# Performance work log

Measured on AMD Instinct MI355X. Metric: run time of the kernel, lower is better.

The kernel has to match this reference:

```python
import jax, jax.numpy as jnp
import numpy as np

L, H, D, HD, DFF, V, S, B = 12, 12, 768, 64, 3072, 50257, 512, 4
NEG = -1e10  # mask value used by the torch module (applied incl. diagonal, pre-scale)


def layer_norm(x, g, b, eps=1e-5):
    u = jnp.mean(x, axis=-1, keepdims=True)
    v = jnp.mean((x - u) ** 2, axis=-1, keepdims=True)  # biased variance
    return g * (x - u) / jnp.sqrt(v + eps) + b


def setup_inputs() -> dict:
    key = jax.random.key(0)
    ks = jax.random.split(key, 10)
    f = lambda k, s: 0.02 * jax.random.normal(k, s, dtype=jnp.float32)
    return {
        "tokens": jax.random.randint(ks[0], (B, S), 0, V),
        "E": f(ks[1], (V, D)),
        "P": f(ks[2], (S, D)),
        "Wq": f(ks[3], (L, H, HD, D)),
        "Wk": f(ks[4], (L, H, HD, D)),
        "Wv": f(ks[5], (L, H, HD, D)),
        "Wo": f(ks[6], (L, D, D)),
        "bo": jnp.zeros((L, D), jnp.float32),
        "g1": jnp.ones((L, D), jnp.float32),
        "b1": jnp.zeros((L, D), jnp.float32),
        "g2": jnp.ones((L, D), jnp.float32),
        "b2": jnp.zeros((L, D), jnp.float32),
        "W1": f(ks[7], (L, DFF, D)),
        "bff1": jnp.zeros((L, DFF), jnp.float32),
        "W2": f(ks[8], (L, D, DFF)),
        "bff2": jnp.zeros((L, D), jnp.float32),
        "gf": jnp.ones((D,), jnp.float32),
        "bf": jnp.zeros((D,), jnp.float32),
    }


def reference(tokens, E, P, Wq, Wk, Wv, Wo, bo, g1, b1, g2, b2, W1, bff1, W2, bff2, gf, bf):
    x = E[tokens] + P[None, :, :]  # [B,S,D]; embed_dropout is identity at eval
    # Faithful mask: triu with diagonal=0 (masks the diagonal too), added BEFORE 1/sqrt(dk)
    mask = jnp.triu(jnp.ones((S, S), jnp.float32), k=0) * NEG
    scale = 1.0 / jnp.sqrt(jnp.float32(HD))
    for l in range(L):
        h = layer_norm(x, g1[l], b1[l])
        Q = jnp.einsum('bsd,hkd->bhsk', h, Wq[l])
        K = jnp.einsum('bsd,hkd->bhsk', h, Wk[l])
        Vh = jnp.einsum('bsd,hkd->bhsk', h, Wv[l])
        sc = (jnp.einsum('bhqk,bhmk->bhqm', Q, K) + mask) * scale  # [B,H,S,S]
        A = jax.nn.softmax(sc, axis=-1)
        o = jnp.einsum('bhqm,bhmk->bhqk', A, Vh)  # [B,H,S,HD]
        o = o.transpose(0, 2, 1, 3).reshape(B, S, D)  # concat heads
        x = x + jnp.einsum('bsd,ed->bse', o, Wo[l]) + bo[l]
        h2 = layer_norm(x, g2[l], b2[l])
        ff = jax.nn.gelu(jnp.einsum('bsd,fd->bsf', h2, W1[l]) + bff1[l], approximate=False)
        x = x + jnp.einsum('bsf,df->bsd', ff, W2[l]) + bff2[l]
    x = layer_norm(x, gf, bf)
    return jnp.einsum('bsd,vd->bsv', x, E)  # weight-tied LM head
```

## Files before the change

### kernel.cpp

```cpp
#include <hip/hip_runtime.h>
#include <hip/hip_bf16.h>
#include <math.h>
#include <stdint.h>

#define L      12
#define H      12
#define DMODEL 768
#define HDIM   64
#define DFF    3072
#define VOCAB  50257
#define VPAD2  50432
#define SEQ    512
#define BATCH  4
#define MTOK   2048
#define BKK    64

typedef __hip_bfloat16 bf16;
typedef __bf16 bf16x8 __attribute__((ext_vector_type(8)));
typedef float  f32x4  __attribute__((ext_vector_type(4)));

__device__ inline unsigned int f2bf_bits(float f) {
    __hip_bfloat16 h = __float2bfloat16(f);
    return (unsigned int)__builtin_bit_cast(unsigned short, h);
}

typedef __attribute__((address_space(1))) unsigned int as1_uint;
typedef __attribute__((address_space(3))) unsigned int as3_uint;

__device__ inline void load_lds_16B(const void* g, void* l) {
    __builtin_amdgcn_global_load_lds((as1_uint*)(uintptr_t)g,
                                     (as3_uint*)(uintptr_t)l, 16, 0, 0);
}

__device__ inline int xcd_swz(int raw, int nwg) {
    return (raw & 7) * (nwg >> 3) + (raw >> 3);
}

struct CvtP {
    const float* src[7];
    bf16* dst[7];
    long ns[7];
    long nt[7];
};

__global__ void cvt_all_kernel(CvtP c) {
    long gid0 = ((long)blockIdx.x * blockDim.x + threadIdx.x) * 8;
    long gstr = (long)gridDim.x * blockDim.x * 8;
    for (int s = 0; s < 7; s++) {
        const float* src = c.src[s];
        bf16* dst = c.dst[s];
        long ns = c.ns[s], ntt = c.nt[s];
        for (long i8 = gid0; i8 < ntt; i8 += gstr) {
            uint4 out;
            if (i8 < ns) {
                float4 a = *reinterpret_cast<const float4*>(src + i8);
                float4 b = *reinterpret_cast<const float4*>(src + i8 + 4);
                out.x = f2bf_bits(a.x) | (f2bf_bits(a.y) << 16);
                out.y = f2bf_bits(a.z) | (f2bf_bits(a.w) << 16);
                out.z = f2bf_bits(b.x) | (f2bf_bits(b.y) << 16);
                out.w = f2bf_bits(b.z) | (f2bf_bits(b.w) << 16);
            } else {
                out = (uint4){0u, 0u, 0u, 0u};
            }
            *reinterpret_cast<uint4*>(dst + i8) = out;
        }
    }
}

__global__ __launch_bounds__(256) void embed_ln_kernel(
        float* __restrict__ x, bf16* __restrict__ hout,
        const int* __restrict__ tok, const float* __restrict__ E,
        const float* __restrict__ Pp, const float* __restrict__ g,
        const float* __restrict__ b) {
    int wave = threadIdx.x >> 6, lane = threadIdx.x & 63;
    int row = blockIdx.x * 4 + wave;
    int s = row & (SEQ - 1);
    long ebase = (long)tok[row] * 192;
    const float4* E4 = (const float4*)E;
    const float4* P4 = (const float4*)Pp;
    float4 v[3];
    float s1 = 0.f, s2 = 0.f;
    #pragma unroll
    for (int e = 0; e < 3; e++) {
        int c4 = e * 64 + lane;
        float4 a = E4[ebase + c4];
        float4 p = P4[s * 192 + c4];
        a.x += p.x; a.y += p.y; a.z += p.z; a.w += p.w;
        v[e] = a;
        ((float4*)x)[(size_t)row * 192 + c4] = a;
        s1 += a.x + a.y + a.z + a.w;
        s2 += a.x * a.x + a.y * a.y + a.z * a.z + a.w * a.w;
    }
    #pragma unroll
    for (int o = 32; o > 0; o >>= 1) {
        s1 += __shfl_xor(s1, o);
        s2 += __shfl_xor(s2, o);
    }
    float u    = s1 * (1.f / DMODEL);
    float var  = s2 * (1.f / DMODEL) - u * u;
    float rstd = rsqrtf(var + 1e-5f);
    #pragma unroll
    for (int e = 0; e < 3; e++) {
        int c4 = e * 64 + lane;
        float4 gg = ((const float4*)g)[c4];
        float4 bb = ((const float4*)b)[c4];
        float y0 = gg.x * (v[e].x - u) * rstd + bb.x;
        float y1 = gg.y * (v[e].y - u) * rstd + bb.y;
        float y2 = gg.z * (v[e].z - u) * rstd + bb.z;
        float y3 = gg.w * (v[e].w - u) * rstd + bb.w;
        uint2 o2;
        o2.x = f2bf_bits(y0) | (f2bf_bits(y1) << 16);
        o2.y = f2bf_bits(y2) | (f2bf_bits(y3) << 16);
        ((uint2*)hout)[(size_t)row * 192 + c4] = o2;
    }
}

__global__ __launch_bounds__(256) void reduce_ln_kernel(
        float* __restrict__ x, const float* __restrict__ part, int S,
        const float* __restrict__ bias, const float* __restrict__ g,
        const float* __restrict__ b, bf16* __restrict__ hout) {
    int wave = threadIdx.x >> 6, lane = threadIdx.x & 63;
    int row = blockIdx.x * 4 + wave;
    const float4* part4 = (const float4*)part;
    float4 v[3];
    float s1 = 0.f, s2 = 0.f;
    #pragma unroll
    for (int e = 0; e < 3; e++) {
        int c4 = e * 64 + lane;
        size_t idx = (size_t)row * 192 + c4;
        float4 a = ((const float4*)x)[idx];
        float4 bi = ((const float4*)bias)[c4];
        a.x += bi.x; a.y += bi.y; a.z += bi.z; a.w += bi.w;
        for (int sl = 0; sl < S; sl++) {
            float4 p = part4[((size_t)sl * MTOK + row) * 192 + c4];
            a.x += p.x; a.y += p.y; a.z += p.z; a.w += p.w;
        }
        v[e] = a;
        ((float4*)x)[idx] = a;
        s1 += a.x + a.y + a.z + a.w;
        s2 += a.x * a.x + a.y * a.y + a.z * a.z + a.w * a.w;
    }
    #pragma unroll
    for (int o = 32; o > 0; o >>= 1) {
        s1 += __shfl_xor(s1, o);
        s2 += __shfl_xor(s2, o);
    }
    float u    = s1 * (1.f / DMODEL);
    float var  = s2 * (1.f / DMODEL) - u * u;
    float rstd = rsqrtf(var + 1e-5f);
    #pragma unroll
    for (int e = 0; e < 3; e++) {
        int c4 = e * 64 + lane;
        float4 gg = ((const float4*)g)[c4];
        float4 bb = ((const float4*)b)[c4];
        float y0 = gg.x * (v[e].x - u) * rstd + bb.x;
        float y1 = gg.y * (v[e].y - u) * rstd + bb.y;
        float y2 = gg.z * (v[e].z - u) * rstd + bb.z;
        float y3 = gg.w * (v[e].w - u) * rstd + bb.w;
        uint2 o2;
        o2.x = f2bf_bits(y0) | (f2bf_bits(y1) << 16);
        o2.y = f2bf_bits(y2) | (f2bf_bits(y3) << 16);
        ((uint2*)hout)[(size_t)row * 192 + c4] = o2;
    }
}

#define BM 128

template<int BN_, int EPI>
__global__ __launch_bounds__(256) void gemm_bt(
    const bf16* __restrict__ A, const bf16* __restrict__ Bmat, long strideBz,
    void* __restrict__ Cout, long strideCz,
    const float* __restrict__ bias,
    int Mm, int Nn, int Kk, int Nstore, int kslice)
{
    constexpr int NF = BN_ / 32;
    __shared__ __align__(16) bf16 As[2][BM * BKK];
    __shared__ __align__(16) bf16 Bs[2][BN_ * BKK];
    int tid = threadIdx.x;
    int lane = tid & 63, wave = tid >> 6;

    int Mtiles = Mm / BM;
    int id = xcd_swz(blockIdx.x, gridDim.x);
    int bm = (id % Mtiles) * BM;
    int bn = (id / Mtiles) * BN_;
    int z = blockIdx.z;
    const bf16* Bz = Bmat + (size_t)z * strideBz;
    int wr = (wave >> 1) * 64, wc = (wave & 1) * (BN_ / 2);

    int k0 = (EPI == 4) ? z * kslice : 0;
    int nt = ((EPI == 4) ? kslice : Kk) / BKK;

    f32x4 acc[4][NF];
    #pragma unroll
    for (int i = 0; i < 4; i++)
        #pragma unroll
        for (int j = 0; j < NF; j++) acc[i][j] = (f32x4){0.f, 0.f, 0.f, 0.f};

    auto stage = [&](int slot, int kt) {
        #pragma unroll
        for (int i = 0; i < 4; i++) {
            int byte = i * 4096 + tid * 16;
            int r = byte >> 7;
            int scb = (byte & 127) ^ ((r & 7) << 4);
            load_lds_16B(A + (size_t)(bm + r) * Kk + kt + (scb >> 1),
                         (char*)As[slot] + byte);
        }
        #pragma unroll
        for (int i = 0; i < BN_ / 32; i++) {
            int byte = i * 4096 + tid * 16;
            int r = byte >> 7;
            int scb = (byte & 127) ^ ((r & 7) << 4);
            load_lds_16B(Bz + (size_t)(bn + r) * Kk + kt + (scb >> 1),
                         (char*)Bs[slot] + byte);
        }
    };

    const int swz_rd = (lane & 7) << 4;
    stage(0, k0);
    for (int t = 0; t < nt; ++t) {
        if (t + 1 < nt) {
            stage((t + 1) & 1, k0 + (t + 1) * BKK);
            if constexpr (BN_ == 128) {
                asm volatile("s_waitcnt vmcnt(8)" ::: "memory");
            } else {
                asm volatile("s_waitcnt vmcnt(6)" ::: "memory");
            }
        } else {
            asm volatile("s_waitcnt vmcnt(0)" ::: "memory");
        }
        __builtin_amdgcn_s_barrier();
        __builtin_amdgcn_sched_barrier(0);
        __builtin_amdgcn_s_setprio(1);
        int cur = t & 1;
        #pragma unroll
        for (int kk = 0; kk < 2; ++kk) {
            bf16x8 af[4], bfr[NF];
            int ro = lane & 15;
            int cob = kk * 64 + (lane >> 4) * 16;
            #pragma unroll
            for (int mi = 0; mi < 4; mi++) {
                int row = wr + mi * 16 + ro;
                af[mi] = *reinterpret_cast<const bf16x8*>(
                    (const char*)As[cur] + row * 128 + (cob ^ swz_rd));
            }
            #pragma unroll
            for (int ni = 0; ni < NF; ni++) {
                int row = wc + ni * 16 + ro;
                bfr[ni] = *reinterpret_cast<const bf16x8*>(
                    (const char*)Bs[cur] + row * 128 + (cob ^ swz_rd));
            }
            #pragma unroll
            for (int mi = 0; mi < 4; mi++)
                #pragma unroll
                for (int ni = 0; ni < NF; ni++)
                    acc[mi][ni] = __builtin_amdgcn_mfma_f32_16x16x32_bf16(
                        af[mi], bfr[ni], acc[mi][ni], 0, 0, 0);
        }
        __builtin_amdgcn_s_setprio(0);
        __builtin_amdgcn_s_barrier();
    }

    int rbase = bm + wr + ((lane >> 4) << 2);
    int cbase = bn + wc + (lane & 15);
    #pragma unroll
    for (int mi = 0; mi < 4; mi++) {
        #pragma unroll
        for (int ni = 0; ni < NF; ni++) {
            int col = cbase + ni * 16;
            #pragma unroll
            for (int r = 0; r < 4; r++) {
                int row = rbase + mi * 16 + r;
                float v = acc[mi][ni][r];
                if constexpr (EPI == 0) {
                    ((bf16*)Cout)[(size_t)z * strideCz + (size_t)row * Nn + col] =
                        __float2bfloat16(v);
                } else if constexpr (EPI == 2) {
                    float t2 = v + bias[col];
                    float gel = 0.5f * t2 * (1.f + erff(t2 * 0.70710678118654752f));
                    ((bf16*)Cout)[(size_t)row * Nn + col] = __float2bfloat16(gel);
                } else if constexpr (EPI == 3) {
                    if (col < Nstore)
                        ((float*)Cout)[(size_t)row * Nstore + col] = v;
                } else {
                    ((float*)Cout)[(size_t)z * strideCz + (size_t)row * Nn + col] = v;
                }
            }
        }
    }
}

#define H8P_READ_A(mq_)                                                        \
    _Pragma("unroll")                                                          \
    for (int mi = 0; mi < 4; mi++) {                                           \
        int row = wm * 64 + mi * 16 + ro;                                      \
        _Pragma("unroll")                                                      \
        for (int kk = 0; kk < 2; kk++) {                                       \
            af[mq_][mi][kk] = *reinterpret_cast<const bf16x8*>(                \
                smem + (slot * 2 + mq_) * 16384 + row * 128 +                  \
                ((kk * 64 + cg16) ^ ((row & 7) << 4)));                        \
        }                                                                      \
    }

#define H8P_READ_B(nq_)                                                       \
    _Pragma("unroll")                                                          \
    for (int ni = 0; ni < 2; ni++) {                                           \
        int row = wn * 32 + ni * 16 + ro;                                      \
        _Pragma("unroll")                                                      \
        for (int kk = 0; kk < 2; kk++) {                                       \
            bfr[nq_][ni][kk] = *reinterpret_cast<const bf16x8*>(               \
                smem + 65536 + (slot * 2 + nq_) * 16384 + row * 128 +          \
                ((kk * 64 + cg16) ^ ((row & 7) << 4)));                        \
        }                                                                      \
    }

#define H8P_MFMA(mq_, nq_)                                                     \
    __builtin_amdgcn_s_setprio(1);                                             \
    _Pragma("unroll")                                                          \
    for (int kk = 0; kk < 2; kk++)                                             \
        _Pragma("unroll")                                                      \
        for (int mi = 0; mi < 4; mi++)                                         \
            _Pragma("unroll")                                                  \
            for (int ni = 0; ni < 2; ni++)                                     \
                acc[mq_][nq_][mi][ni] = __builtin_amdgcn_mfma_f32_16x16x32_bf16( \
                    af[mq_][mi][kk], bfr[nq_][ni][kk], acc[mq_][nq_][mi][ni],  \
                    0, 0, 0);                                                  \
    __builtin_amdgcn_s_setprio(0);

__global__ void __launch_bounds__(512, 2) gemm_head8p(
    const bf16* __restrict__ A, const bf16* __restrict__ Bmat,
    float* __restrict__ Cout, int Nstore)
{
    extern __shared__ char smem[];
    const int Kk = DMODEL;
    const int nt = Kk / BKK;
    int tid = threadIdx.x;
    int lane = tid & 63, wave = tid >> 6;
    int wm = wave >> 2, wn = wave & 3;
    int id = xcd_swz(blockIdx.x, gridDim.x);
    int bm = (id & 7) * 256;
    int bn = (id >> 3) * 256;
    const int ro = lane & 15;
    const int cg16 = (lane >> 4) * 16;

    f32x4 acc[2][2][4][2];
    #pragma unroll
    for (int a0 = 0; a0 < 2; a0++)
        #pragma unroll
        for (int a1 = 0; a1 < 2; a1++)
            #pragma unroll
            for (int a2 = 0; a2 < 4; a2++)
                #pragma unroll
                for (int a3 = 0; a3 < 2; a3++)
                    acc[a0][a1][a2][a3] = (f32x4){0.f, 0.f, 0.f, 0.f};

    bf16x8 af[2][4][2];
    bf16x8 bfr[2][2][2];

    auto stage_half = [&](int slot_, int kt, int which) {
        int h = which >> 1;
        #pragma unroll
        for (int i = 0; i < 2; i++) {
            int byte = i * 8192 + tid * 16;
            int r = byte >> 7;
            int scb = (byte & 127) ^ ((r & 7) << 4);
            if ((which & 1) == 0)
                load_lds_16B(A + (size_t)(bm + h * 128 + r) * Kk + kt + (scb >> 1),
                             smem + (slot_ * 2 + h) * 16384 + byte);
            else
                load_lds_16B(Bmat + (size_t)(bn + h * 128 + r) * Kk + kt + (scb >> 1),
                             smem + 65536 + (slot_ * 2 + h) * 16384 + byte);
        }
    };

    stage_half(0, 0, 0); stage_half(0, 0, 1); stage_half(0, 0, 2); stage_half(0, 0, 3);

    for (int k = 0; k < nt; ++k) {
        int slot = k & 1, nslot = slot ^ 1;
        int kt2 = (k + 1) * BKK;
        bool pf = (k + 1 < nt);

        asm volatile("s_waitcnt vmcnt(4)" ::: "memory");
        if (pf) stage_half(nslot, kt2, 0);
        __builtin_amdgcn_s_barrier();
        __builtin_amdgcn_sched_barrier(0);
        H8P_READ_A(0)
        H8P_READ_B(0)
        asm volatile("s_waitcnt lgkmcnt(0)" ::: "memory");
        __builtin_amdgcn_sched_barrier(0);
        H8P_MFMA(0, 0)

        if (pf) {
            asm volatile("s_waitcnt vmcnt(4)" ::: "memory");
        } else {
            asm volatile("s_waitcnt vmcnt(2)" ::: "memory");
        }
        if (pf) stage_half(nslot, kt2, 1);
        __builtin_amdgcn_s_barrier();
        __builtin_amdgcn_sched_barrier(0);
        H8P_READ_A(1)
        asm volatile("s_waitcnt lgkmcnt(0)" ::: "memory");
        __builtin_amdgcn_sched_barrier(0);
        H8P_MFMA(1, 0)

        if (pf) {
            asm volatile("s_waitcnt vmcnt(4)" ::: "memory");
        } else {
            asm volatile("s_waitcnt vmcnt(0)" ::: "memory");
        }
        if (pf) stage_half(nslot, kt2, 2);
        __builtin_amdgcn_s_barrier();
        __builtin_amdgcn_sched_barrier(0);
        H8P_READ_B(1)
        asm volatile("s_waitcnt lgkmcnt(0)" ::: "memory");
        __builtin_amdgcn_sched_barrier(0);
        H8P_MFMA(0, 1)

        if (pf) stage_half(nslot, kt2, 3);
        __builtin_amdgcn_s_barrier();
        __builtin_amdgcn_sched_barrier(0);
        H8P_MFMA(1, 1)
    }

    #pragma unroll
    for (int mq = 0; mq < 2; mq++) {
        #pragma unroll
        for (int nq = 0; nq < 2; nq++) {
            #pragma unroll
            for (int mi = 0; mi < 4; mi++) {
                #pragma unroll
                for (int ni = 0; ni < 2; ni++) {
                    int col = bn + nq * 128 + wn * 32 + ni * 16 + (lane & 15);
                    #pragma unroll
                    for (int r = 0; r < 4; r++) {
                        int row = bm + mq * 128 + wm * 64 + mi * 16 +
                                  ((lane >> 4) << 2) + r;
                        if (col < Nstore)
                            Cout[(size_t)row * Nstore + col] = acc[mq][nq][mi][ni][r];
                    }
                }
            }
        }
    }
}

#define NEGMASK -1e10f
#define SM_SCALE 0.125f

__global__ __launch_bounds__(256) void attn_kernel(
    bf16* __restrict__ o, const bf16* __restrict__ qb,
    const bf16* __restrict__ kb, const bf16* __restrict__ vb)
{
    __shared__ __align__(16) bf16 K_lds[64 * 64];
    __shared__ __align__(16) bf16 VT_lds[64 * 64];
    __shared__ __align__(16) bf16 P_lds[4][16 * 64];

    int tid = threadIdx.x;
    int wave = tid >> 6, lane = tid & 63;
    int g = lane >> 4;
    int cq = lane & 15;
    int idx = xcd_swz(blockIdx.x, gridDim.x);
    int qt = idx & 7;
    int bh = idx >> 3;
    int h = bh % H, b = bh / H;
    int q0 = qt * 64;
    const size_t base = ((size_t)b * SEQ) * DMODEL + h * HDIM;

    bf16x8 qa[2];
    #pragma unroll
    for (int kk = 0; kk < 2; kk++)
        qa[kk] = *reinterpret_cast<const bf16x8*>(
            qb + base + (size_t)(q0 + wave * 16 + cq) * DMODEL + kk * 32 + g * 8);

    f32x4 acc_o[4];
    #pragma unroll
    for (int df = 0; df < 4; df++) acc_o[df] = (f32x4){0.f, 0.f, 0.f, 0.f};
    float m_run[4] = {-INFINITY, -INFINITY, -INFINITY, -INFINITY};
    float l_run[4] = {0.f, 0.f, 0.f, 0.f};

    int ntiles = (qt == 0) ? (SEQ / 64) : (qt + 1);
    for (int t = 0; t < ntiles; ++t) {
        int mt = t * 64;
        __syncthreads();
        #pragma unroll
        for (int i = 0; i < 2; i++) {
            int byte = i * 4096 + tid * 16;
            int r = byte >> 7;
            int scb = (byte & 127) ^ ((r & 7) << 4);
            load_lds_16B(kb + base + (size_t)(mt + r) * DMODEL + (scb >> 1),
                         (char*)K_lds + byte);
        }
        {
            int rp = tid & 31;
            int c0 = (tid >> 5) * 8;
            const bf16* v0p = vb + base + (size_t)(mt + 2 * rp) * DMODEL + c0;
            uint4 a = *reinterpret_cast<const uint4*>(v0p);
            uint4 bb = *reinterpret_cast<const uint4*>(v0p + DMODEL);
            unsigned int au[4] = {a.x, a.y, a.z, a.w};
            unsigned int bu[4] = {bb.x, bb.y, bb.z, bb.w};
            #pragma unroll
            for (int j = 0; j < 8; j++) {
                unsigned int lo = (j & 1) ? (au[j >> 1] >> 16) : (au[j >> 1] & 0xffffu);
                unsigned int hi = (j & 1) ? (bu[j >> 1] >> 16) : (bu[j >> 1] & 0xffffu);
                int d = c0 + j;
                int byte = d * 128 + ((rp * 4) ^ ((d & 7) << 4));
                *reinterpret_cast<unsigned int*>((char*)VT_lds + byte) = lo | (hi << 16);
            }
        }
        __syncthreads();

        f32x4 s[4];
        #pragma unroll
        for (int nf = 0; nf < 4; nf++) s[nf] = (f32x4){0.f, 0.f, 0.f, 0.f};
        __builtin_amdgcn_s_setprio(1);
        #pragma unroll
        for (int kk = 0; kk < 2; kk++) {
            #pragma unroll
            for (int nf = 0; nf < 4; nf++) {
                int row = nf * 16 + cq;
                bf16x8 kf = *reinterpret_cast<const bf16x8*>(
                    (const char*)K_lds + row * 128 +
                    ((kk * 64 + g * 16) ^ ((row & 7) << 4)));
                s[nf] = __builtin_amdgcn_mfma_f32_16x16x32_bf16(qa[kk], kf, s[nf], 0, 0, 0);
            }
        }
        __builtin_amdgcn_s_setprio(0);

        float p[4][4];
        #pragma unroll
        for (int r = 0; r < 4; r++) {
            int qg = q0 + wave * 16 + (g << 2) + r;
            float sv[4];
            float vmax = -INFINITY;
            #pragma unroll
            for (int nf = 0; nf < 4; nf++) {
                int kv = mt + nf * 16 + cq;
                float d = s[nf][r];
                sv[nf] = (kv >= qg) ? (d + NEGMASK) * SM_SCALE : d * SM_SCALE;
                vmax = fmaxf(vmax, sv[nf]);
            }
            vmax = fmaxf(vmax, __shfl_xor(vmax, 1));
            vmax = fmaxf(vmax, __shfl_xor(vmax, 2));
            vmax = fmaxf(vmax, __shfl_xor(vmax, 4));
            vmax = fmaxf(vmax, __shfl_xor(vmax, 8));
            float nm = fmaxf(m_run[r], vmax);
            float f = __expf(m_run[r] - nm);
            m_run[r] = nm;
            float ps = 0.f;
            #pragma unroll
            for (int nf = 0; nf < 4; nf++) {
                float pv = __expf(sv[nf] - nm);
                p[nf][r] = pv;
                ps += pv;
            }
            ps += __shfl_xor(ps, 1);
            ps += __shfl_xor(ps, 2);
            ps += __shfl_xor(ps, 4);
            ps += __shfl_xor(ps, 8);
            l_run[r] = l_run[r] * f + ps;
            #pragma unroll
            for (int df = 0; df < 4; df++) acc_o[df][r] *= f;
        }

        #pragma unroll
        for (int nf = 0; nf < 4; nf++)
            #pragma unroll
            for (int r = 0; r < 4; r++) {
                int q = (g << 2) + r;
                int blog = nf * 32 + cq * 2;
                int byte = wave * 2048 + q * 128 + (blog ^ ((q & 7) << 4));
                *reinterpret_cast<unsigned short*>((char*)P_lds + byte) =
                    (unsigned short)f2bf_bits(p[nf][r]);
            }
        __syncthreads();

        __builtin_amdgcn_s_setprio(1);
        #pragma unroll
        for (int kk = 0; kk < 2; kk++) {
            bf16x8 pa = *reinterpret_cast<const bf16x8*>(
                (const char*)P_lds + wave * 2048 + cq * 128 +
                ((kk * 64 + g * 16) ^ ((cq & 7) << 4)));
            #pragma unroll
            for (int df = 0; df < 4; df++) {
                int row = df * 16 + cq;
                bf16x8 vf = *reinterpret_cast<const bf16x8*>(
                    (const char*)VT_lds + row * 128 +
                    ((kk * 64 + g * 16) ^ ((row & 7) << 4)));
                acc_o[df] = __builtin_amdgcn_mfma_f32_16x16x32_bf16(pa, vf, acc_o[df], 0, 0, 0);
            }
        }
        __builtin_amdgcn_s_setprio(0);
    }

    #pragma unroll
    for (int r = 0; r < 4; r++) {
        float inv = 1.f / l_run[r];
        int qg = q0 + wave * 16 + (g << 2) + r;
        #pragma unroll
        for (int df = 0; df < 4; df++) {
            o[base + (size_t)qg * DMODEL + df * 16 + cq] =
                __float2bfloat16(acc_o[df][r] * inv);
        }
    }
}

extern "C" void kernel_launch(void* const* d_in, const int* in_sizes, int n_in,
                              void* d_out, int out_size, void* d_ws, size_t ws_size,
                              hipStream_t stream)
{
    (void)in_sizes; (void)n_in; (void)out_size; (void)ws_size;
    const int*   tokens = (const int*)d_in[0];
    const float* E    = (const float*)d_in[1];
    const float* P    = (const float*)d_in[2];
    const float* Wq   = (const float*)d_in[3];
    const float* Wk   = (const float*)d_in[4];
    const float* Wv   = (const float*)d_in[5];
    const float* Wo   = (const float*)d_in[6];
    const float* bo   = (const float*)d_in[7];
    const float* g1   = (const float*)d_in[8];
    const float* b1   = (const float*)d_in[9];
    const float* g2   = (const float*)d_in[10];
    const float* b2   = (const float*)d_in[11];
    const float* W1   = (const float*)d_in[12];
    const float* bff1 = (const float*)d_in[13];
    const float* W2   = (const float*)d_in[14];
    const float* bff2 = (const float*)d_in[15];
    const float* gf   = (const float*)d_in[16];
    const float* bfin = (const float*)d_in[17];

    char* ws = (char*)d_ws;
    size_t off = 0;
    auto alloc = [&](size_t bytes) -> void* {
        void* p = ws + off;
        off += (bytes + 255) & ~(size_t)255;
        return p;
    };
    float* x     = (float*)alloc((size_t)MTOK * DMODEL * 4);
    bf16* hbuf   = (bf16*)alloc((size_t)MTOK * DMODEL * 2);
    bf16* qkv    = (bf16*)alloc((size_t)3 * MTOK * DMODEL * 2);
    bf16* obuf   = (bf16*)alloc((size_t)MTOK * DMODEL * 2);
    bf16* ffb    = (bf16*)alloc((size_t)MTOK * DFF * 2);
    float* part  = (float*)alloc((size_t)3 * MTOK * DMODEL * 4);
    bf16* Eb     = (bf16*)alloc((size_t)VPAD2 * DMODEL * 2);
    bf16* Wqkv_b = (bf16*)alloc((size_t)3 * L * DMODEL * DMODEL * 2);
    bf16* Wo_b   = (bf16*)alloc((size_t)L * DMODEL * DMODEL * 2);
    bf16* W1_b   = (bf16*)alloc((size_t)L * DFF * DMODEL * 2);
    bf16* W2_b   = (bf16*)alloc((size_t)L * DMODEL * DFF * 2);

    long nW = (long)L * DMODEL * DMODEL;
    long nF = (long)L * DFF * DMODEL;
    CvtP cp;
    cp.src[0] = E;  cp.dst[0] = Eb;          cp.ns[0] = (long)VOCAB * DMODEL; cp.nt[0] = (long)VPAD2 * DMODEL;
    cp.src[1] = Wq; cp.dst[1] = Wqkv_b;      cp.ns[1] = nW; cp.nt[1] = nW;
    cp.src[2] = Wk; cp.dst[2] = Wqkv_b + nW; cp.ns[2] = nW; cp.nt[2] = nW;
    cp.src[3] = Wv; cp.dst[3] = Wqkv_b + 2 * nW; cp.ns[3] = nW; cp.nt[3] = nW;
    cp.src[4] = Wo; cp.dst[4] = Wo_b;        cp.ns[4] = nW; cp.nt[4] = nW;
    cp.src[5] = W1; cp.dst[5] = W1_b;        cp.ns[5] = nF; cp.nt[5] = nF;
    cp.src[6] = W2; cp.dst[6] = W2_b;        cp.ns[6] = nF; cp.nt[6] = nF;
    cvt_all_kernel<<<2048, 256, 0, stream>>>(cp);

    embed_ln_kernel<<<MTOK / 4, 256, 0, stream>>>(x, hbuf, tokens, E, P, g1, b1);

    const long pstride = (long)MTOK * DMODEL;
    for (int l = 0; l < L; ++l) {
        gemm_bt<64, 0><<<dim3(192, 1, 3), 256, 0, stream>>>(
            hbuf, Wqkv_b + (size_t)l * DMODEL * DMODEL, nW,
            qkv, pstride, nullptr, MTOK, DMODEL, DMODEL, 0, 0);
        attn_kernel<<<BATCH * H * (SEQ / 64), 256, 0, stream>>>(
            obuf, qkv, qkv + pstride, qkv + 2 * pstride);
        gemm_bt<64, 4><<<dim3(192, 1, 3), 256, 0, stream>>>(
            obuf, Wo_b + (size_t)l * DMODEL * DMODEL, 0,
            part, pstride, nullptr, MTOK, DMODEL, DMODEL, 0, DMODEL / 3);
        reduce_ln_kernel<<<MTOK / 4, 256, 0, stream>>>(
            x, part, 3, bo + l * DMODEL, g2 + l * DMODEL, b2 + l * DMODEL, hbuf);
        gemm_bt<128, 2><<<dim3(16 * 24, 1, 1), 256, 0, stream>>>(
            hbuf, W1_b + (size_t)l * DFF * DMODEL, 0,
            ffb, 0, bff1 + l * DFF, MTOK, DFF, DMODEL, 0, 0);
        gemm_bt<64, 4><<<dim3(192, 1, 3), 256, 0, stream>>>(
            ffb, W2_b + (size_t)l * DMODEL * DFF, 0,
            part, pstride, nullptr, MTOK, DMODEL, DFF, 0, DFF / 3);
        const float* ng = (l < L - 1) ? (g1 + (l + 1) * DMODEL) : gf;
        const float* nb = (l < L - 1) ? (b1 + (l + 1) * DMODEL) : bfin;
        reduce_ln_kernel<<<MTOK / 4, 256, 0, stream>>>(
            x, part, 3, bff2 + l * DMODEL, ng, nb, hbuf);
    }

    (void)hipFuncSetAttribute((const void*)gemm_head8p,
        hipFuncAttributeMaxDynamicSharedMemorySize, 131072);
    (void)hipGetLastError();
    gemm_head8p<<<dim3(8 * 197), 512, 131072, stream>>>(
        hbuf, Eb, (float*)d_out, VOCAB);
    if (hipGetLastError() != hipSuccess) {
        gemm_bt<128, 3><<<dim3(16 * 394, 1, 1), 256, 0, stream>>>(
            hbuf, Eb, 0, d_out, 0, nullptr, MTOK, VPAD2, DMODEL, VOCAB, 0);
    }
}
```

Before: 1.703 ms.

## Double-buffer K tiles and register-prefetch V in attention loop

The attention kernel now keeps two K tiles in LDS and loads V for the next tile into registers during the current iteration, so global loads overlap with compute. The full __syncthreads calls are replaced by explicit vmcnt/lgkmcnt waits plus raw s_barrier and sched_barrier, cutting the per-tile barrier count. The aim is to hide the global-memory latency of K/V staging. In exchange it uses more LDS and registers, and correctness now depends on hand-tuned waitcnt counts.

```diff
diff --git a/kernel.cpp b/kernel.cpp
--- a/kernel.cpp
+++ b/kernel.cpp
@@ -450,7 +450,7 @@
     bf16* __restrict__ o, const bf16* __restrict__ qb,
     const bf16* __restrict__ kb, const bf16* __restrict__ vb)
 {
-    __shared__ __align__(16) bf16 K_lds[64 * 64];
+    __shared__ __align__(16) bf16 K_lds[2][64 * 64];
     __shared__ __align__(16) bf16 VT_lds[64 * 64];
     __shared__ __align__(16) bf16 P_lds[4][16 * 64];
 
@@ -471,32 +471,54 @@
         qa[kk] = *reinterpret_cast<const bf16x8*>(
             qb + base + (size_t)(q0 + wave * 16 + cq) * DMODEL + kk * 32 + g * 8);
 
-    f32x4 acc_o[4];
-    #pragma unroll
-    for (int df = 0; df < 4; df++) acc_o[df] = (f32x4){0.f, 0.f, 0.f, 0.f};
-    float m_run[4] = {-INFINITY, -INFINITY, -INFINITY, -INFINITY};
-    float l_run[4] = {0.f, 0.f, 0.f, 0.f};
-
-    int ntiles = (qt == 0) ? (SEQ / 64) : (qt + 1);
-    for (int t = 0; t < ntiles; ++t) {
-        int mt = t * 64;
-        __syncthreads();
+    int rp = tid & 31;
+    int c0 = (tid >> 5) * 8;
+    const bf16* vbase = vb + base + (size_t)(2 * rp) * DMODEL + c0;
+
+    auto stageK = [&](int slot, int mt) {
         #pragma unroll
         for (int i = 0; i < 2; i++) {
             int byte = i * 4096 + tid * 16;
             int r = byte >> 7;
             int scb = (byte & 127) ^ ((r & 7) << 4);
             load_lds_16B(kb + base + (size_t)(mt + r) * DMODEL + (scb >> 1),
-                         (char*)K_lds + byte);
-        }
+                         (char*)K_lds[slot] + byte);
+        }
+    };
+
+    f32x4 acc_o[4];
+    #pragma unroll
+    for (int df = 0; df < 4; df++) acc_o[df] = (f32x4){0.f, 0.f, 0.f, 0.f};
+    float m_run[4] = {-INFINITY, -INFINITY, -INFINITY, -INFINITY};
+    float l_run[4] = {0.f, 0.f, 0.f, 0.f};
+
+    int ntiles = (qt == 0) ? (SEQ / 64) : (qt + 1);
+
+    stageK(0, 0);
+    uint4 vA = *reinterpret_cast<const uint4*>(vbase);
+    uint4 vB = *reinterpret_cast<const uint4*>(vbase + DMODEL);
+    asm volatile("s_waitcnt vmcnt(0)" ::: "memory");
+
+    for (int t = 0; t < ntiles; ++t) {
+        int mt = t * 64;
+        int s = t & 1;
+        uint4 nvA, nvB;
+        bool pf = (t + 1 < ntiles);
+        if (pf) {
+            stageK(s ^ 1, mt + 64);
+            const bf16* nv = vbase + (size_t)(mt + 64) * DMODEL;
+            nvA = *reinterpret_cast<const uint4*>(nv);
+            nvB = *reinterpret_cast<const uint4*>(nv + DMODEL);
+            asm volatile("s_waitcnt vmcnt(4)" ::: "memory");
+        } else {
+            asm volatile("s_waitcnt vmcnt(0)" ::: "memory");
+        }
+        __builtin_amdgcn_s_barrier();
+        __builtin_amdgcn_sched_barrier(0);
+
         {
-            int rp = tid & 31;
-            int c0 = (tid >> 5) * 8;
-            const bf16* v0p = vb + base + (size_t)(mt + 2 * rp) * DMODEL + c0;
-            uint4 a = *reinterpret_cast<const uint4*>(v0p);
-            uint4 bb = *reinterpret_cast<const uint4*>(v0p + DMODEL);
-            unsigned int au[4] = {a.x, a.y, a.z, a.w};
-            unsigned int bu[4] = {bb.x, bb.y, bb.z, bb.w};
+            unsigned int au[4] = {vA.x, vA.y, vA.z, vA.w};
+            unsigned int bu[4] = {vB.x, vB.y, vB.z, vB.w};
             #pragma unroll
             for (int j = 0; j < 8; j++) {
                 unsigned int lo = (j & 1) ? (au[j >> 1] >> 16) : (au[j >> 1] & 0xffffu);
@@ -506,11 +528,10 @@
                 *reinterpret_cast<unsigned int*>((char*)VT_lds + byte) = lo | (hi << 16);
             }
         }
-        __syncthreads();
-
-        f32x4 s[4];
-        #pragma unroll
-        for (int nf = 0; nf < 4; nf++) s[nf] = (f32x4){0.f, 0.f, 0.f, 0.f};
+
+        f32x4 sc[4];
+        #pragma unroll
+        for (int nf = 0; nf < 4; nf++) sc[nf] = (f32x4){0.f, 0.f, 0.f, 0.f};
         __builtin_amdgcn_s_setprio(1);
         #pragma unroll
         for (int kk = 0; kk < 2; kk++) {
@@ -518,9 +539,9 @@
             for (int nf = 0; nf < 4; nf++) {
                 int row = nf * 16 + cq;
                 bf16x8 kf = *reinterpret_cast<const bf16x8*>(
-                    (const char*)K_lds + row * 128 +
+                    (const char*)K_lds[s] + row * 128 +
                     ((kk * 64 + g * 16) ^ ((row & 7) << 4)));
-                s[nf] = __builtin_amdgcn_mfma_f32_16x16x32_bf16(qa[kk], kf, s[nf], 0, 0, 0);
+                sc[nf] = __builtin_amdgcn_mfma_f32_16x16x32_bf16(qa[kk], kf, sc[nf], 0, 0, 0);
             }
         }
         __builtin_amdgcn_s_setprio(0);
@@ -534,7 +555,7 @@
             #pragma unroll
             for (int nf = 0; nf < 4; nf++) {
                 int kv = mt + nf * 16 + cq;
-                float d = s[nf][r];
+                float d = sc[nf][r];
                 sv[nf] = (kv >= qg) ? (d + NEGMASK) * SM_SCALE : d * SM_SCALE;
                 vmax = fmaxf(vmax, sv[nf]);
             }
@@ -571,7 +592,9 @@
                 *reinterpret_cast<unsigned short*>((char*)P_lds + byte) =
                     (unsigned short)f2bf_bits(p[nf][r]);
             }
-        __syncthreads();
+        asm volatile("s_waitcnt lgkmcnt(0)" ::: "memory");
+        __builtin_amdgcn_s_barrier();
+        __builtin_amdgcn_sched_barrier(0);
 
         __builtin_amdgcn_s_setprio(1);
         #pragma unroll
@@ -589,6 +612,8 @@
             }
         }
         __builtin_amdgcn_s_setprio(0);
+
+        if (pf) { vA = nvA; vB = nvB; }
     }
 
     #pragma unroll
```

New measurement: 1.700 ms (median of 2 runs). Within noise of the previous version (-0.2%).
